# Performance work log

Measured on AMD Instinct MI355X. Metric: run time of the kernel, lower is better.

## Reference

```python
import jax, jax.numpy as jnp
import numpy as np

ROPE_BASE = 10000
B, L, D, NH = 2, 2048, 1024, 16
HD = D // NH


def apply_rope(inputs, positions, base_frequency):
    # inputs: [B, L, N, H], positions: [L]
    head_dim = inputs.shape[-1]
    fraction = 2 * jnp.arange(0, head_dim // 2) / head_dim
    timescale = base_frequency ** fraction  # [H/2]
    sinusoid = positions[..., None] / timescale[None, None, :]  # [1, L, H/2]
    sinusoid = sinusoid[..., None, :]  # [1, L, 1, H/2]
    sin, cos = jnp.sin(sinusoid), jnp.cos(sinusoid)
    first, second = jnp.split(inputs, 2, axis=-1)
    out = jnp.concatenate([first * cos - second * sin,
                           second * cos + first * sin], axis=-1)
    return out.astype(inputs.dtype)


def setup_inputs() -> dict:
    key = jax.random.key(0)
    ks = jax.random.split(key, 5)
    s = 0.02
    return {
        "x": jax.random.normal(ks[0], (B, L, D), jnp.float32),
        "wq_w": jax.random.normal(ks[1], (D, D), jnp.float32) * s,
        "wq_b": jnp.zeros((D,), jnp.float32),
        "wk_w": jax.random.normal(ks[2], (D, D), jnp.float32) * s,
        "wk_b": jnp.zeros((D,), jnp.float32),
        "wv_w": jax.random.normal(ks[3], (D, D), jnp.float32) * s,
        "wv_b": jnp.zeros((D,), jnp.float32),
        "wo_w": jax.random.normal(ks[4], (D, D), jnp.float32) * s,
        "wo_b": jnp.zeros((D,), jnp.float32),
    }


def reference(x, wq_w, wq_b, wk_w, wk_b, wv_w, wv_b, wo_w, wo_b):
    b, l, _ = x.shape
    q = (x @ wq_w + wq_b).reshape(b, l, NH, HD)
    k = (x @ wk_w + wk_b).reshape(b, l, NH, HD)
    v = (x @ wv_w + wv_b).reshape(b, l, NH, HD)
    pos = jnp.arange(l)
    q = apply_rope(q, pos, ROPE_BASE)
    k = apply_rope(k, pos, ROPE_BASE)
    # [B, N, L, H]
    q = q.transpose(0, 2, 1, 3)
    k = k.transpose(0, 2, 1, 3)
    v = v.transpose(0, 2, 1, 3)
    scale = jnp.sqrt(jnp.asarray(HD, q.dtype))
    scores = jnp.einsum('bnqh,bnkh->bnqk', q, k) / scale  # [B, N, L, L]
    causal = jnp.tril(jnp.ones((l, l), bool))
    scores = jnp.where(causal, scores, jnp.finfo(scores.dtype).min)
    attn = jax.nn.softmax(scores, axis=-1)
    ctx = jnp.einsum('bnqk,bnkh->bnqh', attn, v)
    ctx = ctx.transpose(0, 2, 1, 3).reshape(b, l, D)
    return ctx @ wo_w + wo_b
```

## Files before the change

### kernel.cpp

```cpp
#include <hip/hip_runtime.h>
#include <hip/hip_bf16.h>
#include <float.h>
#include <math.h>

#define BB  2
#define LLEN 2048
#define DD  1024
#define NHH 16
#define HDD 64
#define MROWS (BB * LLEN)

typedef __bf16 bf16x8  __attribute__((ext_vector_type(8)));
typedef float  f32x4   __attribute__((ext_vector_type(4)));
typedef float  f32x16  __attribute__((ext_vector_type(16)));

#define EXP2F(x) __builtin_amdgcn_exp2f(x)

static __device__ __forceinline__ ushort f2bf(float f) {
    __hip_bfloat16 h = __float2bfloat16(f);
    return *reinterpret_cast<ushort*>(&h);
}
static __device__ __forceinline__ unsigned pack2(float a, float b) {
    return (unsigned)f2bf(a) | ((unsigned)f2bf(b) << 16);
}

__device__ __forceinline__ void gload16(const void* g, void* l) {
    __builtin_amdgcn_global_load_lds(
        (const __attribute__((address_space(1))) void*)g,
        (__attribute__((address_space(3))) void*)l, 16, 0, 0);
}

__global__ __launch_bounds__(256) void cvt_x_k(const float* __restrict__ in,
                                               ushort* __restrict__ out) {
    int idx = blockIdx.x * 256 + threadIdx.x;
    float4 v = reinterpret_cast<const float4*>(in)[idx];
    ushort4 o;
    o.x = f2bf(v.x); o.y = f2bf(v.y); o.z = f2bf(v.z); o.w = f2bf(v.w);
    reinterpret_cast<ushort4*>(out)[idx] = o;
}

__global__ __launch_bounds__(256) void wt_cvt_all_k(const float* __restrict__ w0,
                                                    const float* __restrict__ w1,
                                                    const float* __restrict__ w2,
                                                    const float* __restrict__ w3,
                                                    ushort* __restrict__ qkv,
                                                    ushort* __restrict__ wo) {
    __shared__ float T[64][65];
    const int z = blockIdx.z;
    const float* in = (z == 0) ? w0 : (z == 1) ? w1 : (z == 2) ? w2 : w3;
    ushort* out = (z < 3) ? (qkv + (size_t)z * 1024 * DD) : wo;

    const int r0 = blockIdx.y * 64, c0 = blockIdx.x * 64;
    const int tid = threadIdx.x;
    for (int i = tid; i < 64 * 16; i += 256) {
        int r = i >> 4, c4 = (i & 15) * 4;
        float4 v = *reinterpret_cast<const float4*>(&in[(size_t)(r0 + r) * DD + c0 + c4]);
        T[r][c4 + 0] = v.x; T[r][c4 + 1] = v.y; T[r][c4 + 2] = v.z; T[r][c4 + 3] = v.w;
    }
    __syncthreads();
    for (int i = tid; i < 64 * 16; i += 256) {
        int rr = i >> 4, cc4 = (i & 15) * 4;
        ushort4 o;
        o.x = f2bf(T[cc4 + 0][rr]);
        o.y = f2bf(T[cc4 + 1][rr]);
        o.z = f2bf(T[cc4 + 2][rr]);
        o.w = f2bf(T[cc4 + 3][rr]);
        *reinterpret_cast<ushort4*>(&out[(size_t)(c0 + rr) * DD + r0 + cc4]) = o;
    }
}

template <int MODE>
__global__ __launch_bounds__(256) void gemm_mfma_k(
    const __bf16* __restrict__ A, const __bf16* __restrict__ Bt,
    const float* __restrict__ bias0, const float* __restrict__ bias1,
    const float* __restrict__ bias2,
    float* __restrict__ out_f32,
    __hip_bfloat16* __restrict__ oq, __hip_bfloat16* __restrict__ ok,
    __hip_bfloat16* __restrict__ ov) {
    constexpr int K = DD;
    __shared__ __bf16 As[128 * 64];
    __shared__ __bf16 Bs[128 * 64];

    const int tid  = threadIdx.x;
    const int w    = tid >> 6;
    const int lane = tid & 63;
    const int lr   = lane & 15;
    const int lg   = lane >> 4;
    const int wr   = w >> 1, wc = w & 1;
    const int bm = blockIdx.y * 128, bn = blockIdx.x * 128;

    const int srow = lane >> 3;
    const int scol = ((lane & 7) ^ srow) * 8;
    const __bf16* gA = A  + (size_t)(bm + w * 32 + srow) * K + scol;
    const __bf16* gB = Bt + (size_t)(bn + w * 32 + srow) * K + scol;
    char* ldsA = (char*)As + w * 32 * 128;
    char* ldsB = (char*)Bs + w * 32 * 128;

    f32x4 acc[4][4] = {};

    const int l7 = lr & 7;
    for (int k0 = 0; k0 < K; k0 += 64) {
#pragma unroll
        for (int c = 0; c < 4; ++c) {
            gload16(gA + (size_t)(c * 8) * K + k0, ldsA + c * 1024);
            gload16(gB + (size_t)(c * 8) * K + k0, ldsB + c * 1024);
        }
        __syncthreads();
#pragma unroll
        for (int kk = 0; kk < 2; ++kk) {
            bf16x8 a[4], b[4];
#pragma unroll
            for (int m = 0; m < 4; ++m)
                a[m] = *reinterpret_cast<const bf16x8*>(
                    As + (wr * 64 + m * 16 + lr) * 64 + (((kk * 4 + lg) ^ l7) << 3));
#pragma unroll
            for (int n = 0; n < 4; ++n)
                b[n] = *reinterpret_cast<const bf16x8*>(
                    Bs + (wc * 64 + n * 16 + lr) * 64 + (((kk * 4 + lg) ^ l7) << 3));
#pragma unroll
            for (int m = 0; m < 4; ++m)
#pragma unroll
                for (int n = 0; n < 4; ++n)
                    acc[m][n] = __builtin_amdgcn_mfma_f32_16x16x32_bf16(a[m], b[n], acc[m][n], 0, 0, 0);
        }
        __syncthreads();
    }

    if (MODE == 1) {
        const int seg = bn >> 10;
        const int colbase = (bn & 1023) + wc * 64;
        const int h = colbase >> 6;
        if (seg == 2) {
#pragma unroll
            for (int n = 0; n < 4; ++n) {
                const int hd = n * 16 + lr;
                const float bv = bias2[colbase + hd];
#pragma unroll
                for (int m = 0; m < 4; ++m) {
                    const int rowb = bm + wr * 64 + m * 16 + lg * 4;
                    const int b = rowb >> 11, l0 = rowb & (LLEN - 1);
                    ushort4 st;
                    st.x = f2bf(acc[m][n][0] + bv);
                    st.y = f2bf(acc[m][n][1] + bv);
                    st.z = f2bf(acc[m][n][2] + bv);
                    st.w = f2bf(acc[m][n][3] + bv);
                    const int bh = b * NHH + h;
                    const int t  = l0 >> 5;
                    const int j  = ((hd >> 5) << 1) | ((l0 >> 4) & 1);
                    const int ln = (hd & 31) + ((l0 >> 3) & 1) * 32;
                    const int e0 = l0 & 7;
                    size_t base = ((((size_t)bh * 64 + t) * 4 + j) * 64 + ln) * 8 + e0;
                    *reinterpret_cast<ushort4*>(&ov[base]) = st;
                }
            }
        } else {
            const float* biasp = (seg == 0) ? bias0 : bias1;
            const float osc = (seg == 0) ? 0.18033688011112042f : 1.0f;
#pragma unroll
            for (int n2 = 0; n2 < 2; ++n2) {
                const int d = n2 * 16 + lr;
                const float tsd = exp2f((float)d * -0.4152410118609203f);
                const float bv0 = biasp[colbase + d];
                const float bv1 = biasp[colbase + d + 32];
#pragma unroll
                for (int m = 0; m < 4; ++m) {
                    const int rowb = bm + wr * 64 + m * 16 + lg * 4;
                    const int b = rowb >> 11, lb = rowb & (LLEN - 1);
#pragma unroll
                    for (int i = 0; i < 4; ++i) {
                        const int l = lb + i;
                        float s, c;
                        __sincosf((float)l * tsd, &s, &c);
                        const float x0 = (acc[m][n2][i] + bv0);
                        const float x1 = (acc[m][n2 + 2][i] + bv1);
                        const float r0 = (x0 * c - x1 * s) * osc;
                        const float r1 = (x1 * c + x0 * s) * osc;
                        if (seg == 0) {
                            __hip_bfloat16* pb =
                                oq + ((size_t)(b * NHH + h) * LLEN + l) * HDD;
                            pb[d]      = __float2bfloat16(r0);
                            pb[d + 32] = __float2bfloat16(r1);
                        } else {
                            const int bh = b * NHH + h;
                            const int t  = l >> 5;
                            const int c_ = d >> 4;
                            const int ln = (l & 31) + ((d >> 3) & 1) * 32;
                            size_t base = ((((size_t)bh * 64 + t) * 4 + c_) * 64 + ln) * 8 + (d & 7);
                            ok[base]            = __float2bfloat16(r0);
                            ok[base + 2 * 512]  = __float2bfloat16(r1);
                        }
                    }
                }
            }
        }
    } else {
#pragma unroll
        for (int n = 0; n < 4; ++n) {
            const int gn = bn + wc * 64 + n * 16 + lr;
            const float bv = bias0[gn];
#pragma unroll
            for (int m = 0; m < 4; ++m)
#pragma unroll
                for (int i = 0; i < 4; ++i) {
                    const int row = bm + wr * 64 + m * 16 + lg * 4 + i;
                    out_f32[(size_t)row * DD + gn] = acc[m][n][i] + bv;
                }
        }
    }
}

#define ATTN_LOAD(KF, VF, T0)                                                   \
    do {                                                                        \
        const __bf16* kp_ = kbase + (size_t)(T0) * 2048;                        \
        KF[0] = *reinterpret_cast<const bf16x8*>(kp_);                          \
        KF[1] = *reinterpret_cast<const bf16x8*>(kp_ + 512);                    \
        KF[2] = *reinterpret_cast<const bf16x8*>(kp_ + 1024);                   \
        KF[3] = *reinterpret_cast<const bf16x8*>(kp_ + 1536);                   \
        const __bf16* vp_ = vbase + (size_t)(T0) * 2048;                        \
        VF[0] = *reinterpret_cast<const bf16x8*>(vp_);                          \
        VF[1] = *reinterpret_cast<const bf16x8*>(vp_ + 512);                    \
        VF[2] = *reinterpret_cast<const bf16x8*>(vp_ + 1024);                   \
        VF[3] = *reinterpret_cast<const bf16x8*>(vp_ + 1536);                   \
    } while (0)

#define ATTN_TILE(KF, VF, T0, MASKIT, QG)                                       \
    do {                                                                        \
        f32x16 s_ = {};                                                         \
        __builtin_amdgcn_s_setprio(1);                                          \
        s_ = __builtin_amdgcn_mfma_f32_32x32x16_bf16(KF[0], qf[0], s_, 0, 0, 0);\
        s_ = __builtin_amdgcn_mfma_f32_32x32x16_bf16(KF[1], qf[1], s_, 0, 0, 0);\
        s_ = __builtin_amdgcn_mfma_f32_32x32x16_bf16(KF[2], qf[2], s_, 0, 0, 0);\
        s_ = __builtin_amdgcn_mfma_f32_32x32x16_bf16(KF[3], qf[3], s_, 0, 0, 0);\
        __builtin_amdgcn_s_setprio(0);                                          \
        float p_[16];                                                           \
        const int k0_ = (T0) * 32;                                              \
        if (MASKIT) {                                                           \
            _Pragma("unroll")                                                   \
            for (int i = 0; i < 16; ++i) {                                      \
                int kkg_ = k0_ + (i & 3) + 8 * (i >> 2) + 4 * hi;               \
                p_[i] = (kkg_ <= (QG)) ? EXP2F(s_[i]) : 0.f;                    \
            }                                                                   \
        } else {                                                                \
            _Pragma("unroll")                                                   \
            for (int i = 0; i < 16; ++i) p_[i] = EXP2F(s_[i]);                  \
        }                                                                       \
        _Pragma("unroll")                                                       \
        for (int i = 0; i < 16; ++i) lsum += p_[i];                             \
        unsigned u_[8], x_[8];                                                  \
        _Pragma("unroll")                                                       \
        for (int j = 0; j < 8; ++j)                                             \
            u_[j] = pack2(p_[2 * j], p_[2 * j + 1]);                            \
        _Pragma("unroll")                                                       \
        for (int j = 0; j < 8; ++j)                                             \
            x_[j] = (unsigned)__shfl_xor((int)u_[j], 32);                       \
        union { unsigned d[4]; bf16x8 v; } B1_, B2_;                            \
        if (hi == 0) {                                                          \
            B1_.d[0] = u_[0]; B1_.d[1] = u_[1]; B1_.d[2] = x_[0]; B1_.d[3] = x_[1]; \
            B2_.d[0] = u_[4]; B2_.d[1] = u_[5]; B2_.d[2] = x_[4]; B2_.d[3] = x_[5]; \
        } else {                                                                \
            B1_.d[0] = x_[2]; B1_.d[1] = x_[3]; B1_.d[2] = u_[2]; B1_.d[3] = u_[3]; \
            B2_.d[0] = x_[6]; B2_.d[1] = x_[7]; B2_.d[2] = u_[6]; B2_.d[3] = u_[7]; \
        }                                                                       \
        __builtin_amdgcn_s_setprio(1);                                          \
        o0 = __builtin_amdgcn_mfma_f32_32x32x16_bf16(VF[0], B1_.v, o0, 0, 0, 0);\
        o0 = __builtin_amdgcn_mfma_f32_32x32x16_bf16(VF[1], B2_.v, o0, 0, 0, 0);\
        o1 = __builtin_amdgcn_mfma_f32_32x32x16_bf16(VF[2], B1_.v, o1, 0, 0, 0);\
        o1 = __builtin_amdgcn_mfma_f32_32x32x16_bf16(VF[3], B2_.v, o1, 0, 0, 0);\
        __builtin_amdgcn_s_setprio(0);                                          \
    } while (0)

#define ATTN_COMPUTE(QT, QG)                                                    \
    do {                                                                        \
        lsum = 0.f;                                                             \
        o0 = (f32x16){}; o1 = (f32x16){};                                       \
        _Pragma("unroll")                                                       \
        for (int d = 0; d < 4; ++d)                                             \
            qf[d] = *reinterpret_cast<const bf16x8*>(                           \
                Qh + (size_t)(QG) * HDD + d * 16 + hi * 8);                     \
        bf16x8 kf[4], vf[4];                                                    \
        for (int t = w; t <= (QT); t += 4) {                                    \
            ATTN_LOAD(kf, vf, t);                                               \
            ATTN_TILE(kf, vf, t, t == (QT), QG);                                \
        }                                                                       \
    } while (0)

#define ATTN_WRITE_PARTIALS()                                                   \
    do {                                                                        \
        _Pragma("unroll")                                                       \
        for (int r = 0; r < 16; ++r) {                                          \
            oL[w][lane][r]      = o0[r];                                        \
            oL[w][lane][16 + r] = o1[r];                                        \
        }                                                                       \
        lvL[w][lane] = lsum;                                                    \
    } while (0)

#define ATTN_MERGE_WRITE(QG)                                                    \
    do {                                                                        \
        float Lt = 0.f;                                                         \
        _Pragma("unroll")                                                       \
        for (int j = 0; j < 4; ++j)                                             \
            Lt += lvL[j][q32] + lvL[j][q32 + 32];                               \
        const float inv = 1.0f / Lt;                                            \
        __hip_bfloat16* dst = ctx + ((size_t)(b * LLEN + (QG))) * DD + h * HDD; \
        const int T = w >> 1;                                                   \
        const int gb = (w & 1) * 2;                                             \
        _Pragma("unroll")                                                       \
        for (int g2 = 0; g2 < 2; ++g2) {                                        \
            const int g = gb + g2;                                              \
            ushort st4[4];                                                      \
            _Pragma("unroll")                                                   \
            for (int e = 0; e < 4; ++e) {                                       \
                const int r = T * 16 + 4 * g + e;                               \
                float val = oL[0][lane][r] + oL[1][lane][r] +                   \
                            oL[2][lane][r] + oL[3][lane][r];                    \
                st4[e] = f2bf(val * inv);                                       \
            }                                                                   \
            const int d = T * 32 + 8 * g + 4 * hi;                              \
            *reinterpret_cast<ushort4*>(dst + d) =                              \
                *reinterpret_cast<ushort4*>(st4);                               \
        }                                                                       \
    } while (0)

__global__ __launch_bounds__(256) void attn_mfma13_k(const __bf16* __restrict__ Q,
                                                     const __bf16* __restrict__ Kp,
                                                     const __bf16* __restrict__ Vp,
                                                     __hip_bfloat16* __restrict__ ctx) {
    __shared__ float oL[4][64][33];
    __shared__ float lvL[4][64];

    const int tid  = threadIdx.x;
    const int w    = tid >> 6;
    const int lane = tid & 63;
    const int q32  = lane & 31;
    const int hi   = lane >> 5;

    const int bid = blockIdx.x;
    const int g_  = (bid & 7) * 128 + (bid >> 3);
    const int bh  = g_ >> 5;
    const int ap  = g_ & 31;
    const int qtA = 63 - ap;
    const int qtB = ap;
    const int qgA = qtA * 32 + q32;
    const int qgB = qtB * 32 + q32;

    const __bf16* Qh = Q + (size_t)bh * LLEN * HDD;
    const __bf16* kbase = Kp + (size_t)bh * (64 * 4 * 512) + lane * 8;
    const __bf16* vbase = Vp + (size_t)bh * (64 * 4 * 512) + lane * 8;

    const int b = bh >> 4, h = bh & 15;

    bf16x8 qf[4];
    f32x16 o0, o1;
    float lsum;

    ATTN_COMPUTE(qtA, qgA);
    ATTN_WRITE_PARTIALS();
    __syncthreads();
    ATTN_MERGE_WRITE(qgA);

    ATTN_COMPUTE(qtB, qgB);
    __syncthreads();
    ATTN_WRITE_PARTIALS();
    __syncthreads();
    ATTN_MERGE_WRITE(qgB);
}

extern "C" void kernel_launch(void* const* d_in, const int* in_sizes, int n_in,
                              void* d_out, int out_size, void* d_ws, size_t ws_size,
                              hipStream_t stream) {
    const float* x    = (const float*)d_in[0];
    const float* wq_w = (const float*)d_in[1];
    const float* wq_b = (const float*)d_in[2];
    const float* wk_w = (const float*)d_in[3];
    const float* wk_b = (const float*)d_in[4];
    const float* wv_w = (const float*)d_in[5];
    const float* wv_b = (const float*)d_in[6];
    const float* wo_w = (const float*)d_in[7];
    const float* wo_b = (const float*)d_in[8];
    float* out = (float*)d_out;

    const size_t MB = 1024 * 1024;
    char* p = (char*)d_ws;
    __bf16* x16   = (__bf16*)p;            p += 8 * MB;
    __bf16* wqkvt = (__bf16*)p;            p += 6 * MB;
    __bf16* wot   = (__bf16*)p;            p += 2 * MB;
    __hip_bfloat16* q16  = (__hip_bfloat16*)p; p += 8 * MB;
    __hip_bfloat16* kp16 = (__hip_bfloat16*)p; p += 8 * MB;
    __hip_bfloat16* vp16 = (__hip_bfloat16*)p; p += 8 * MB;
    __hip_bfloat16* ctx16 = (__hip_bfloat16*)p;

    hipLaunchKernelGGL(cvt_x_k, dim3(4096), dim3(256), 0, stream, x, (ushort*)x16);
    hipLaunchKernelGGL(wt_cvt_all_k, dim3(16, 16, 4), dim3(256), 0, stream,
                       wq_w, wk_w, wv_w, wo_w, (ushort*)wqkvt, (ushort*)wot);

    hipLaunchKernelGGL((gemm_mfma_k<1>), dim3(24, 32), dim3(256), 0, stream,
                       x16, wqkvt, wq_b, wk_b, wv_b, (float*)nullptr, q16, kp16, vp16);

    hipLaunchKernelGGL(attn_mfma13_k, dim3(1024), dim3(256), 0, stream,
                       (const __bf16*)q16, (const __bf16*)kp16, (const __bf16*)vp16, ctx16);

    hipLaunchKernelGGL((gemm_mfma_k<0>), dim3(8, 32), dim3(256), 0, stream,
                       (const __bf16*)ctx16, wot, wo_b, (const float*)nullptr, (const float*)nullptr,
                       out, (__hip_bfloat16*)nullptr, (__hip_bfloat16*)nullptr, (__hip_bfloat16*)nullptr);
}
```

Measured before the change: 110.5 us.

## Stage GEMM epilogues through LDS for coalesced stores; pack Q in MFMA layout

The QKV GEMM epilogue now writes RoPE'd Q and K into per-wave LDS tiles in the packed fragment layout, then copies them to global memory with 16-byte coalesced stores. Q now uses the same packed layout as K, so the attention kernel loads Q fragments with the same strided vector loads as K and V. The output projection epilogue also stages fp32 results through LDS to emit float4 row stores instead of scattered scalar stores. This adds __syncthreads and LDS traffic to the epilogues in exchange for fewer, wider global writes.

```diff
diff --git a/kernel.cpp b/kernel.cpp
--- a/kernel.cpp
+++ b/kernel.cpp
@@ -13,6 +13,7 @@
 typedef __bf16 bf16x8  __attribute__((ext_vector_type(8)));
 typedef float  f32x4   __attribute__((ext_vector_type(4)));
 typedef float  f32x16  __attribute__((ext_vector_type(16)));
+typedef ushort us8     __attribute__((ext_vector_type(8)));
 
 #define EXP2F(x) __builtin_amdgcn_exp2f(x)
 
@@ -78,8 +79,9 @@
     __hip_bfloat16* __restrict__ oq, __hip_bfloat16* __restrict__ ok,
     __hip_bfloat16* __restrict__ ov) {
     constexpr int K = DD;
-    __shared__ __bf16 As[128 * 64];
-    __shared__ __bf16 Bs[128 * 64];
+    __shared__ char smem[32768];
+    __bf16* As = (__bf16*)smem;
+    __bf16* Bs = As + 128 * 64;
 
     const int tid  = threadIdx.x;
     const int w    = tid >> 6;
@@ -156,55 +158,79 @@
         } else {
             const float* biasp = (seg == 0) ? bias0 : bias1;
             const float osc = (seg == 0) ? 0.18033688011112042f : 1.0f;
+            ushort* LP = (ushort*)smem + (size_t)w * 4096;
+            __syncthreads();
 #pragma unroll
             for (int n2 = 0; n2 < 2; ++n2) {
                 const int d = n2 * 16 + lr;
                 const float tsd = exp2f((float)d * -0.4152410118609203f);
                 const float bv0 = biasp[colbase + d];
                 const float bv1 = biasp[colbase + d + 32];
+                const int c0  = d >> 4;
+                const int hi8 = (d >> 3) & 1;
 #pragma unroll
                 for (int m = 0; m < 4; ++m) {
-                    const int rowb = bm + wr * 64 + m * 16 + lg * 4;
-                    const int b = rowb >> 11, lb = rowb & (LLEN - 1);
 #pragma unroll
                     for (int i = 0; i < 4; ++i) {
-                        const int l = lb + i;
+                        const int lw = m * 16 + lg * 4 + i;
+                        const int lglob = (bm & (LLEN - 1)) + wr * 64 + lw;
                         float s, c;
-                        __sincosf((float)l * tsd, &s, &c);
-                        const float x0 = (acc[m][n2][i] + bv0);
-                        const float x1 = (acc[m][n2 + 2][i] + bv1);
-                        const float r0 = (x0 * c - x1 * s) * osc;
-                        const float r1 = (x1 * c + x0 * s) * osc;
-                        if (seg == 0) {
-                            __hip_bfloat16* pb =
-                                oq + ((size_t)(b * NHH + h) * LLEN + l) * HDD;
-                            pb[d]      = __float2bfloat16(r0);
-                            pb[d + 32] = __float2bfloat16(r1);
-                        } else {
-                            const int bh = b * NHH + h;
-                            const int t  = l >> 5;
-                            const int c_ = d >> 4;
-                            const int ln = (l & 31) + ((d >> 3) & 1) * 32;
-                            size_t base = ((((size_t)bh * 64 + t) * 4 + c_) * 64 + ln) * 8 + (d & 7);
-                            ok[base]            = __float2bfloat16(r0);
-                            ok[base + 2 * 512]  = __float2bfloat16(r1);
-                        }
+                        __sincosf((float)lglob * tsd, &s, &c);
+                        const float x0 = acc[m][n2][i] + bv0;
+                        const float x1 = acc[m][n2 + 2][i] + bv1;
+                        const int tt = lw >> 5;
+                        const int ln = (lw & 31) + 32 * hi8;
+                        LP[(((tt << 2) + c0) * 64 + ln) * 8 + (d & 7)] =
+                            f2bf((x0 * c - x1 * s) * osc);
+                        LP[(((tt << 2) + c0 + 2) * 64 + ln) * 8 + (d & 7)] =
+                            f2bf((x1 * c + x0 * s) * osc);
                     }
                 }
             }
+            __syncthreads();
+            ushort* dstp = (ushort*)((seg == 0) ? oq : ok);
+            const int bh0 = (bm >> 11) * NHH + h;
+            const int tg0 = ((bm & (LLEN - 1)) >> 5) + wr * 2;
+#pragma unroll
+            for (int tt = 0; tt < 2; ++tt)
+#pragma unroll
+                for (int c = 0; c < 4; ++c) {
+                    us8 v = *reinterpret_cast<const us8*>(
+                        &LP[(((tt << 2) + c) * 64 + lane) * 8]);
+                    size_t base = ((((size_t)bh0 * 64 + tg0 + tt) * 4 + c) * 64 + lane) * 8;
+                    *reinterpret_cast<us8*>(&dstp[base]) = v;
+                }
         }
     } else {
-#pragma unroll
-        for (int n = 0; n < 4; ++n) {
-            const int gn = bn + wc * 64 + n * 16 + lr;
-            const float bv = bias0[gn];
-#pragma unroll
-            for (int m = 0; m < 4; ++m)
-#pragma unroll
-                for (int i = 0; i < 4; ++i) {
-                    const int row = bm + wr * 64 + m * 16 + lg * 4 + i;
-                    out_f32[(size_t)row * DD + gn] = acc[m][n][i] + bv;
+        float* FP = (float*)smem + (size_t)w * 2048;
+#pragma unroll
+        for (int ph = 0; ph < 2; ++ph) {
+            __syncthreads();
+#pragma unroll
+            for (int m2 = 0; m2 < 2; ++m2) {
+                const int m = ph * 2 + m2;
+#pragma unroll
+                for (int n = 0; n < 4; ++n) {
+                    const int col = n * 16 + lr;
+                    const float bv = bias0[bn + wc * 64 + col];
+#pragma unroll
+                    for (int i = 0; i < 4; ++i) {
+                        const int rw = m2 * 16 + lg * 4 + i;
+                        FP[rw * 64 + col] = acc[m][n][i] + bv;
+                    }
                 }
+            }
+            __syncthreads();
+#pragma unroll
+            for (int it = 0; it < 8; ++it) {
+                const int idx = it * 64 + lane;
+                const int rw = idx >> 4;
+                const int cq = idx & 15;
+                float4 v = *reinterpret_cast<const float4*>(&FP[rw * 64 + cq * 4]);
+                const int row = bm + wr * 64 + ph * 32 + rw;
+                *reinterpret_cast<float4*>(
+                    &out_f32[(size_t)row * DD + bn + wc * 64 + cq * 4]) = v;
+            }
         }
     }
 }
@@ -273,10 +299,11 @@
     do {                                                                        \
         lsum = 0.f;                                                             \
         o0 = (f32x16){}; o1 = (f32x16){};                                       \
-        _Pragma("unroll")                                                       \
-        for (int d = 0; d < 4; ++d)                                             \
-            qf[d] = *reinterpret_cast<const bf16x8*>(                           \
-                Qh + (size_t)(QG) * HDD + d * 16 + hi * 8);                     \
+        const __bf16* qp_ = qbase + (size_t)(QT) * 2048;                        \
+        qf[0] = *reinterpret_cast<const bf16x8*>(qp_);                          \
+        qf[1] = *reinterpret_cast<const bf16x8*>(qp_ + 512);                    \
+        qf[2] = *reinterpret_cast<const bf16x8*>(qp_ + 1024);                   \
+        qf[3] = *reinterpret_cast<const bf16x8*>(qp_ + 1536);                   \
         bf16x8 kf[4], vf[4];                                                    \
         for (int t = w; t <= (QT); t += 4) {                                    \
             ATTN_LOAD(kf, vf, t);                                               \
@@ -321,7 +348,7 @@
         }                                                                       \
     } while (0)
 
-__global__ __launch_bounds__(256) void attn_mfma13_k(const __bf16* __restrict__ Q,
+__global__ __launch_bounds__(256) void attn_mfma14_k(const __bf16* __restrict__ Qp,
                                                      const __bf16* __restrict__ Kp,
                                                      const __bf16* __restrict__ Vp,
                                                      __hip_bfloat16* __restrict__ ctx) {
@@ -343,7 +370,7 @@
     const int qgA = qtA * 32 + q32;
     const int qgB = qtB * 32 + q32;
 
-    const __bf16* Qh = Q + (size_t)bh * LLEN * HDD;
+    const __bf16* qbase = Qp + (size_t)bh * (64 * 4 * 512) + lane * 8;
     const __bf16* kbase = Kp + (size_t)bh * (64 * 4 * 512) + lane * 8;
     const __bf16* vbase = Vp + (size_t)bh * (64 * 4 * 512) + lane * 8;
 
@@ -384,7 +411,7 @@
     __bf16* x16   = (__bf16*)p;            p += 8 * MB;
     __bf16* wqkvt = (__bf16*)p;            p += 6 * MB;
     __bf16* wot   = (__bf16*)p;            p += 2 * MB;
-    __hip_bfloat16* q16  = (__hip_bfloat16*)p; p += 8 * MB;
+    __hip_bfloat16* qp16 = (__hip_bfloat16*)p; p += 8 * MB;
     __hip_bfloat16* kp16 = (__hip_bfloat16*)p; p += 8 * MB;
     __hip_bfloat16* vp16 = (__hip_bfloat16*)p; p += 8 * MB;
     __hip_bfloat16* ctx16 = (__hip_bfloat16*)p;
@@ -394,10 +421,10 @@
                        wq_w, wk_w, wv_w, wo_w, (ushort*)wqkvt, (ushort*)wot);
 
     hipLaunchKernelGGL((gemm_mfma_k<1>), dim3(24, 32), dim3(256), 0, stream,
-                       x16, wqkvt, wq_b, wk_b, wv_b, (float*)nullptr, q16, kp16, vp16);
-
-    hipLaunchKernelGGL(attn_mfma13_k, dim3(1024), dim3(256), 0, stream,
-                       (const __bf16*)q16, (const __bf16*)kp16, (const __bf16*)vp16, ctx16);
+                       x16, wqkvt, wq_b, wk_b, wv_b, (float*)nullptr, qp16, kp16, vp16);
+
+    hipLaunchKernelGGL(attn_mfma14_k, dim3(1024), dim3(256), 0, stream,
+                       (const __bf16*)qp16, (const __bf16*)kp16, (const __bf16*)vp16, ctx16);
 
     hipLaunchKernelGGL((gemm_mfma_k<0>), dim3(8, 32), dim3(256), 0, stream,
                        (const __bf16*)ctx16, wot, wo_b, (const float*)nullptr, (const float*)nullptr,
```

Result: no change. 109.9 us (-0.5%).
